# Performance work log

Measured on AMD Instinct MI355X. Metric: run time of the kernel, lower is better.

Reference implementation:

```python
import jax, jax.numpy as jnp
import numpy as np

N_NODES = 100000


def setup_inputs() -> dict:
    key = jax.random.key(0)
    ks = jax.random.split(key, 7)
    feats = jax.random.normal(ks[0], (N_NODES, 128), dtype=jnp.float32)
    src = jax.random.randint(ks[1], (1000000,), 0, N_NODES)
    dst = jax.random.randint(ks[2], (1000000,), 0, N_NODES)
    W1 = jax.random.normal(ks[3], (128, 128), dtype=jnp.float32) * (1.0 / np.sqrt(128))
    b1 = jnp.zeros((128,), dtype=jnp.float32)
    W2 = jax.random.normal(ks[4], (128, 40), dtype=jnp.float32) * (1.0 / np.sqrt(128))
    b2 = jnp.zeros((40,), dtype=jnp.float32)
    return {"feats": feats, "src": src, "dst": dst, "W1": W1, "b1": b1, "W2": W2, "b2": b2}


def _sage_gcn_layer(h, src, dst, deg, W, b):
    # DGL SAGEConv aggregator_type='gcn':
    #   neigh = sum over in-edges of src features; h = (neigh + h_self) / (in_deg + 1); out = h @ W + b
    neigh = jax.ops.segment_sum(h[src], dst, num_segments=N_NODES)  # [N, d]
    agg = (neigh + h) / (deg[:, None] + 1.0)
    return agg @ W + b


def reference(feats, src, dst, W1, b1, W2, b2):
    deg = jax.ops.segment_sum(jnp.ones_like(dst, dtype=feats.dtype), dst, num_segments=N_NODES)
    h1 = jax.nn.relu(_sage_gcn_layer(feats, src, dst, deg, W1, b1))  # dropout = identity (eval)
    h2 = _sage_gcn_layer(h1, src, dst, deg, W2, b2)
    # original returns (h_list, h); h_list = [h1, h2], final h = h2
    return (h1, h2)
```

## Files before the change

kernel.cpp:

```cpp
#include <hip/hip_runtime.h>

static inline int ceil_div(int a, int b){ return (a+b-1)/b; }

__global__ __launch_bounds__(256) void k_hist(const int* __restrict__ dst, int E, int* __restrict__ cnt){
  int e = blockIdx.x*256 + threadIdx.x;
  if (e < E) atomicAdd(&cnt[dst[e]], 1);
}

__global__ __launch_bounds__(256) void k_scan_a(const int* __restrict__ cnt, int N, int* __restrict__ bsum){
  __shared__ int s[256];
  int t = threadIdx.x;
  int i0 = blockIdx.x*512 + 2*t;
  int a = (i0   < N) ? cnt[i0]   : 0;
  int b = (i0+1 < N) ? cnt[i0+1] : 0;
  s[t] = a + b;
  __syncthreads();
  for (int off=128; off>0; off>>=1){ if (t<off) s[t]+=s[t+off]; __syncthreads(); }
  if (t==0) bsum[blockIdx.x] = s[0];
}

__global__ __launch_bounds__(256) void k_scan_b(int* __restrict__ bsum, int nb){
  __shared__ int s[256];
  int t = threadIdx.x;
  int v0=0,v1=0,v2=0,v3=0;
  int i0 = t*4;
  if (i0   < nb) v0 = bsum[i0];
  if (i0+1 < nb) v1 = bsum[i0+1];
  if (i0+2 < nb) v2 = bsum[i0+2];
  if (i0+3 < nb) v3 = bsum[i0+3];
  int tsum = v0+v1+v2+v3;
  s[t] = tsum;
  __syncthreads();
  for (int off=1; off<256; off<<=1){
    int v = (t>=off) ? s[t-off] : 0;
    __syncthreads();
    s[t] += v;
    __syncthreads();
  }
  int excl = s[t] - tsum;
  if (i0   < nb) bsum[i0]   = excl;
  if (i0+1 < nb) bsum[i0+1] = excl + v0;
  if (i0+2 < nb) bsum[i0+2] = excl + v0 + v1;
  if (i0+3 < nb) bsum[i0+3] = excl + v0 + v1 + v2;
}

__global__ __launch_bounds__(256) void k_scan_c(const int* __restrict__ cnt, int N,
                                                const int* __restrict__ bsum, int* __restrict__ offs){
  __shared__ int s[256];
  int t = threadIdx.x;
  int i0 = blockIdx.x*512 + 2*t;
  int a = (i0   < N) ? cnt[i0]   : 0;
  int b = (i0+1 < N) ? cnt[i0+1] : 0;
  int tsum = a+b;
  s[t] = tsum;
  __syncthreads();
  for (int off=1; off<256; off<<=1){
    int v = (t>=off) ? s[t-off] : 0;
    __syncthreads();
    s[t] += v;
    __syncthreads();
  }
  int excl = s[t] - tsum + bsum[blockIdx.x];
  if (i0   < N) offs[i0]   = excl;
  if (i0+1 < N) offs[i0+1] = excl + a;
}

__global__ __launch_bounds__(256) void k_place(const int* __restrict__ src, const int* __restrict__ dst, int E,
                                               const int* __restrict__ offs, int* __restrict__ cursor,
                                               int* __restrict__ ss){
  int e = blockIdx.x*256 + threadIdx.x;
  if (e < E){
    int d = dst[e];
    int p = atomicAdd(&cursor[d], 1);
    ss[offs[d] + p] = src[e];
  }
}

__global__ __launch_bounds__(256) void k_agg1(const float* __restrict__ feats,
    const int* __restrict__ ss, const int* __restrict__ offs, const int* __restrict__ cnt,
    float* __restrict__ aggout, int N){
  int w = (int)((blockIdx.x*256u + threadIdx.x) >> 6);
  int lane = threadIdx.x & 63;
  if (w >= N) return;
  int beg = __builtin_amdgcn_readfirstlane(offs[w]);
  int c   = __builtin_amdgcn_readfirstlane(cnt[w]);
  const float2* f2 = (const float2*)feats;
  float2 acc = f2[(size_t)w*64 + lane];
  int i = 0;
  for (; i+4 <= c; i += 4){
    int s0 = ss[beg+i], s1 = ss[beg+i+1], s2 = ss[beg+i+2], s3 = ss[beg+i+3];
    float2 a = f2[(size_t)s0*64 + lane];
    float2 b = f2[(size_t)s1*64 + lane];
    float2 cc= f2[(size_t)s2*64 + lane];
    float2 d = f2[(size_t)s3*64 + lane];
    acc.x += (a.x + b.x) + (cc.x + d.x);
    acc.y += (a.y + b.y) + (cc.y + d.y);
  }
  for (; i < c; ++i){
    int s0 = ss[beg+i];
    float2 a = f2[(size_t)s0*64 + lane];
    acc.x += a.x; acc.y += a.y;
  }
  float inv = 1.0f / (float)(c + 1);
  float2 o; o.x = acc.x*inv; o.y = acc.y*inv;
  ((float2*)aggout)[(size_t)w*64 + lane] = o;
}

__global__ __launch_bounds__(256) void k_gemm1(float* __restrict__ h1,
    const float* __restrict__ W1, const float* __restrict__ b1, int N){
  __shared__ float sA[64*132];
  __shared__ float sW[32*128];
  int t = threadIdx.x;
  int r0 = blockIdx.x*64;
  for (int it=0; it<8; ++it){
    int flat = it*1024 + t*4;
    int r = flat>>7, d = flat&127;
    float4 v = make_float4(0.f,0.f,0.f,0.f);
    if (r0+r < N) v = *(const float4*)(h1 + (size_t)(r0+r)*128 + d);
    *(float4*)&sA[r*132 + d] = v;
  }
  int rg = t>>4, cg = t&15;
  float acc[4][8];
#pragma unroll
  for (int i=0;i<4;++i)
#pragma unroll
    for (int j=0;j<8;++j) acc[i][j]=0.f;

  for (int kc=0; kc<4; ++kc){
    __syncthreads();
#pragma unroll
    for (int it=0; it<4; ++it){
      int flat = it*1024 + t*4;
      *(float4*)&sW[flat] = *(const float4*)(W1 + kc*4096 + flat);
    }
    __syncthreads();
#pragma unroll 4
    for (int dd=0; dd<32; ++dd){
      int d = kc*32 + dd;
      float4 w0 = *(const float4*)&sW[dd*128 + cg*4];
      float4 w1 = *(const float4*)&sW[dd*128 + 64 + cg*4];
      float a0 = sA[(rg   )*132 + d];
      float a1 = sA[(rg+16)*132 + d];
      float a2 = sA[(rg+32)*132 + d];
      float a3 = sA[(rg+48)*132 + d];
      acc[0][0]+=a0*w0.x; acc[0][1]+=a0*w0.y; acc[0][2]+=a0*w0.z; acc[0][3]+=a0*w0.w;
      acc[0][4]+=a0*w1.x; acc[0][5]+=a0*w1.y; acc[0][6]+=a0*w1.z; acc[0][7]+=a0*w1.w;
      acc[1][0]+=a1*w0.x; acc[1][1]+=a1*w0.y; acc[1][2]+=a1*w0.z; acc[1][3]+=a1*w0.w;
      acc[1][4]+=a1*w1.x; acc[1][5]+=a1*w1.y; acc[1][6]+=a1*w1.z; acc[1][7]+=a1*w1.w;
      acc[2][0]+=a2*w0.x; acc[2][1]+=a2*w0.y; acc[2][2]+=a2*w0.z; acc[2][3]+=a2*w0.w;
      acc[2][4]+=a2*w1.x; acc[2][5]+=a2*w1.y; acc[2][6]+=a2*w1.z; acc[2][7]+=a2*w1.w;
      acc[3][0]+=a3*w0.x; acc[3][1]+=a3*w0.y; acc[3][2]+=a3*w0.z; acc[3][3]+=a3*w0.w;
      acc[3][4]+=a3*w1.x; acc[3][5]+=a3*w1.y; acc[3][6]+=a3*w1.z; acc[3][7]+=a3*w1.w;
    }
  }
  float4 bb0 = *(const float4*)(b1 + cg*4);
  float4 bb1 = *(const float4*)(b1 + 64 + cg*4);
#pragma unroll
  for (int i=0;i<4;++i){
    int r = r0 + rg + i*16;
    if (r < N){
      float4 o0, o1;
      o0.x = fmaxf(acc[i][0]+bb0.x, 0.f); o0.y = fmaxf(acc[i][1]+bb0.y, 0.f);
      o0.z = fmaxf(acc[i][2]+bb0.z, 0.f); o0.w = fmaxf(acc[i][3]+bb0.w, 0.f);
      o1.x = fmaxf(acc[i][4]+bb1.x, 0.f); o1.y = fmaxf(acc[i][5]+bb1.y, 0.f);
      o1.z = fmaxf(acc[i][6]+bb1.z, 0.f); o1.w = fmaxf(acc[i][7]+bb1.w, 0.f);
      *(float4*)(h1 + (size_t)r*128 + cg*4)      = o0;
      *(float4*)(h1 + (size_t)r*128 + 64 + cg*4) = o1;
    }
  }
}

__global__ __launch_bounds__(256) void k_gemm2(const float* __restrict__ h1,
    const float* __restrict__ W2, float* __restrict__ t1, int N){
  __shared__ float sA[64*132];
  __shared__ float sW[128*40];
  int t = threadIdx.x;
  int r0 = blockIdx.x*64;
  for (int it=0; it<8; ++it){
    int flat = it*1024 + t*4;
    int r = flat>>7, d = flat&127;
    float4 v = make_float4(0.f,0.f,0.f,0.f);
    if (r0+r < N) v = *(const float4*)(h1 + (size_t)(r0+r)*128 + d);
    *(float4*)&sA[r*132 + d] = v;
  }
#pragma unroll
  for (int it=0; it<5; ++it){
    int flat = it*1024 + t*4;
    *(float4*)&sW[flat] = *(const float4*)(W2 + flat);
  }
  __syncthreads();
  int rg = t>>3, cg = t&7;
  float acc[2][5];
#pragma unroll
  for (int i=0;i<2;++i)
#pragma unroll
    for (int j=0;j<5;++j) acc[i][j]=0.f;
#pragma unroll 4
  for (int d=0; d<128; ++d){
    float a0 = sA[(rg   )*132 + d];
    float a1 = sA[(rg+32)*132 + d];
#pragma unroll
    for (int jj=0;jj<5;++jj){
      float wv = sW[d*40 + cg + 8*jj];
      acc[0][jj] += a0*wv;
      acc[1][jj] += a1*wv;
    }
  }
#pragma unroll
  for (int i=0;i<2;++i){
    int r = r0 + rg + i*32;
    if (r < N){
#pragma unroll
      for (int jj=0;jj<5;++jj) t1[(size_t)r*40 + cg + 8*jj] = acc[i][jj];
    }
  }
}

__global__ __launch_bounds__(256) void k_agg2(const float* __restrict__ t1,
    const int* __restrict__ ss, const int* __restrict__ offs, const int* __restrict__ cnt,
    const float* __restrict__ b2, float* __restrict__ h2, int N){
  int w = (int)((blockIdx.x*256u + threadIdx.x) >> 6);
  int lane = threadIdx.x & 63;
  if (w >= N) return;
  int beg = __builtin_amdgcn_readfirstlane(offs[w]);
  int c   = __builtin_amdgcn_readfirstlane(cnt[w]);
  int l = (lane < 40) ? lane : 0;
  float acc = t1[(size_t)w*40 + l];
  int i = 0;
  for (; i+4 <= c; i += 4){
    int s0 = ss[beg+i], s1 = ss[beg+i+1], s2 = ss[beg+i+2], s3 = ss[beg+i+3];
    float a = t1[(size_t)s0*40 + l];
    float b = t1[(size_t)s1*40 + l];
    float cc= t1[(size_t)s2*40 + l];
    float d = t1[(size_t)s3*40 + l];
    acc += (a + b) + (cc + d);
  }
  for (; i < c; ++i) acc += t1[(size_t)ss[beg+i]*40 + l];
  float inv = 1.0f / (float)(c + 1);
  if (lane < 40) h2[(size_t)w*40 + lane] = acc*inv + b2[lane];
}

extern "C" void kernel_launch(void* const* d_in, const int* in_sizes, int n_in,
                              void* d_out, int out_size, void* d_ws, size_t ws_size,
                              hipStream_t stream){
  const float* feats = (const float*)d_in[0];
  const int*   src   = (const int*)d_in[1];
  const int*   dst   = (const int*)d_in[2];
  const float* W1    = (const float*)d_in[3];
  const float* b1    = (const float*)d_in[4];
  const float* W2    = (const float*)d_in[5];
  const float* b2    = (const float*)d_in[6];
  int N = in_sizes[0] / 128;
  int E = in_sizes[1];
  float* h1 = (float*)d_out;
  float* h2 = h1 + (size_t)N*128;

  size_t need = 0;
  auto lay = [&](size_t bytes)->size_t{ size_t p = need; need += (bytes + 511) & ~(size_t)511; return p; };
  size_t o_cnt    = lay((size_t)N*4);
  size_t o_offs   = lay((size_t)N*4);
  size_t o_cursor = lay((size_t)N*4);
  size_t o_bsum   = lay(4096);
  size_t o_ss     = lay((size_t)E*4);
  size_t o_t1     = lay((size_t)N*40*4);
  if (need > ws_size) return;

  char* wp = (char*)d_ws;
  int*   cnt    = (int*)(wp + o_cnt);
  int*   offs   = (int*)(wp + o_offs);
  int*   cursor = (int*)(wp + o_cursor);
  int*   bsum   = (int*)(wp + o_bsum);
  int*   ss     = (int*)(wp + o_ss);
  float* t1     = (float*)(wp + o_t1);

  hipMemsetAsync(cnt,    0, (size_t)N*4, stream);
  hipMemsetAsync(cursor, 0, (size_t)N*4, stream);

  int nb = ceil_div(N, 512);
  k_hist  <<<ceil_div(E,256), 256, 0, stream>>>(dst, E, cnt);
  k_scan_a<<<nb,              256, 0, stream>>>(cnt, N, bsum);
  k_scan_b<<<1,               256, 0, stream>>>(bsum, nb);
  k_scan_c<<<nb,              256, 0, stream>>>(cnt, N, bsum, offs);
  k_place <<<ceil_div(E,256), 256, 0, stream>>>(src, dst, E, offs, cursor, ss);

  k_agg1  <<<ceil_div(N,4),   256, 0, stream>>>(feats, ss, offs, cnt, h1, N);
  k_gemm1 <<<ceil_div(N,64),  256, 0, stream>>>(h1, W1, b1, N);
  k_gemm2 <<<ceil_div(N,64),  256, 0, stream>>>(h1, W2, t1, N);
  k_agg2  <<<ceil_div(N,4),   256, 0, stream>>>(t1, ss, offs, cnt, b2, h2, N);
}
```

Baseline: 413.3 us.

## Fuse the two GEMMs, drop the cursor array, widen layer-1 gather to float4

k_place now bumps the offsets array atomically, so the separate cursor buffer and its memset go away; the aggregation kernels recover each segment's start as offs minus count. k_agg1 gathers with float4 loads, with each half-wave handling alternate edges and a shuffle merging the two halves. k_gemm1 and k_gemm2 become one kernel that keeps the relu'd h1 tile in shared memory for the second product, which avoids re-reading h1 from global memory. The cost is more shared-memory reuse and a less regular tail in the gather loop.

```diff
diff --git a/kernel.cpp b/kernel.cpp
--- a/kernel.cpp
+++ b/kernel.cpp
@@ -66,13 +66,12 @@
 }
 
 __global__ __launch_bounds__(256) void k_place(const int* __restrict__ src, const int* __restrict__ dst, int E,
-                                               const int* __restrict__ offs, int* __restrict__ cursor,
-                                               int* __restrict__ ss){
+                                               int* __restrict__ offs, int* __restrict__ ss){
   int e = blockIdx.x*256 + threadIdx.x;
   if (e < E){
     int d = dst[e];
-    int p = atomicAdd(&cursor[d], 1);
-    ss[offs[d] + p] = src[e];
+    int p = atomicAdd(&offs[d], 1);
+    ss[p] = src[e];
   }
 }
 
@@ -82,34 +81,58 @@
   int w = (int)((blockIdx.x*256u + threadIdx.x) >> 6);
   int lane = threadIdx.x & 63;
   if (w >= N) return;
-  int beg = __builtin_amdgcn_readfirstlane(offs[w]);
   int c   = __builtin_amdgcn_readfirstlane(cnt[w]);
-  const float2* f2 = (const float2*)feats;
-  float2 acc = f2[(size_t)w*64 + lane];
+  int beg = __builtin_amdgcn_readfirstlane(offs[w]) - c;
+  const float4* f4 = (const float4*)feats;
+  int half = lane >> 5;
+  int qc   = lane & 31;
+  float4 acc = make_float4(0.f,0.f,0.f,0.f);
   int i = 0;
-  for (; i+4 <= c; i += 4){
-    int s0 = ss[beg+i], s1 = ss[beg+i+1], s2 = ss[beg+i+2], s3 = ss[beg+i+3];
-    float2 a = f2[(size_t)s0*64 + lane];
-    float2 b = f2[(size_t)s1*64 + lane];
-    float2 cc= f2[(size_t)s2*64 + lane];
-    float2 d = f2[(size_t)s3*64 + lane];
+  for (; i+8 <= c; i += 8){
+    int i0 = ss[beg+i  +half];
+    int i1 = ss[beg+i+2+half];
+    int i2 = ss[beg+i+4+half];
+    int i3 = ss[beg+i+6+half];
+    float4 a = f4[(size_t)i0*32 + qc];
+    float4 b = f4[(size_t)i1*32 + qc];
+    float4 cc= f4[(size_t)i2*32 + qc];
+    float4 d = f4[(size_t)i3*32 + qc];
     acc.x += (a.x + b.x) + (cc.x + d.x);
     acc.y += (a.y + b.y) + (cc.y + d.y);
-  }
-  for (; i < c; ++i){
-    int s0 = ss[beg+i];
-    float2 a = f2[(size_t)s0*64 + lane];
-    acc.x += a.x; acc.y += a.y;
-  }
-  float inv = 1.0f / (float)(c + 1);
-  float2 o; o.x = acc.x*inv; o.y = acc.y*inv;
-  ((float2*)aggout)[(size_t)w*64 + lane] = o;
-}
-
-__global__ __launch_bounds__(256) void k_gemm1(float* __restrict__ h1,
-    const float* __restrict__ W1, const float* __restrict__ b1, int N){
+    acc.z += (a.z + b.z) + (cc.z + d.z);
+    acc.w += (a.w + b.w) + (cc.w + d.w);
+  }
+  for (; i+2 <= c; i += 2){
+    int i0 = ss[beg+i+half];
+    float4 a = f4[(size_t)i0*32 + qc];
+    acc.x += a.x; acc.y += a.y; acc.z += a.z; acc.w += a.w;
+  }
+  acc.x += __shfl_down(acc.x, 32, 64);
+  acc.y += __shfl_down(acc.y, 32, 64);
+  acc.z += __shfl_down(acc.z, 32, 64);
+  acc.w += __shfl_down(acc.w, 32, 64);
+  if (lane < 32){
+    if (i < c){
+      int i0 = ss[beg+i];
+      float4 a = f4[(size_t)i0*32 + qc];
+      acc.x += a.x; acc.y += a.y; acc.z += a.z; acc.w += a.w;
+    }
+    float4 s = f4[(size_t)w*32 + qc];
+    float inv = 1.0f / (float)(c + 1);
+    float4 o;
+    o.x = (acc.x + s.x) * inv;
+    o.y = (acc.y + s.y) * inv;
+    o.z = (acc.z + s.z) * inv;
+    o.w = (acc.w + s.w) * inv;
+    ((float4*)aggout)[(size_t)w*32 + qc] = o;
+  }
+}
+
+__global__ __launch_bounds__(256) void k_gemm12(float* __restrict__ h1,
+    const float* __restrict__ W1, const float* __restrict__ b1,
+    const float* __restrict__ W2, float* __restrict__ t1, int N){
   __shared__ float sA[64*132];
-  __shared__ float sW[32*128];
+  __shared__ float sW[5120];
   int t = threadIdx.x;
   int r0 = blockIdx.x*64;
   for (int it=0; it<8; ++it){
@@ -153,35 +176,25 @@
       acc[3][4]+=a3*w1.x; acc[3][5]+=a3*w1.y; acc[3][6]+=a3*w1.z; acc[3][7]+=a3*w1.w;
     }
   }
+  __syncthreads();
+
   float4 bb0 = *(const float4*)(b1 + cg*4);
   float4 bb1 = *(const float4*)(b1 + 64 + cg*4);
 #pragma unroll
   for (int i=0;i<4;++i){
-    int r = r0 + rg + i*16;
+    int rr = rg + i*16;
+    int r  = r0 + rr;
+    float4 o0, o1;
+    o0.x = fmaxf(acc[i][0]+bb0.x, 0.f); o0.y = fmaxf(acc[i][1]+bb0.y, 0.f);
+    o0.z = fmaxf(acc[i][2]+bb0.z, 0.f); o0.w = fmaxf(acc[i][3]+bb0.w, 0.f);
+    o1.x = fmaxf(acc[i][4]+bb1.x, 0.f); o1.y = fmaxf(acc[i][5]+bb1.y, 0.f);
+    o1.z = fmaxf(acc[i][6]+bb1.z, 0.f); o1.w = fmaxf(acc[i][7]+bb1.w, 0.f);
+    *(float4*)&sA[rr*132 + cg*4]      = o0;
+    *(float4*)&sA[rr*132 + 64 + cg*4] = o1;
     if (r < N){
-      float4 o0, o1;
-      o0.x = fmaxf(acc[i][0]+bb0.x, 0.f); o0.y = fmaxf(acc[i][1]+bb0.y, 0.f);
-      o0.z = fmaxf(acc[i][2]+bb0.z, 0.f); o0.w = fmaxf(acc[i][3]+bb0.w, 0.f);
-      o1.x = fmaxf(acc[i][4]+bb1.x, 0.f); o1.y = fmaxf(acc[i][5]+bb1.y, 0.f);
-      o1.z = fmaxf(acc[i][6]+bb1.z, 0.f); o1.w = fmaxf(acc[i][7]+bb1.w, 0.f);
       *(float4*)(h1 + (size_t)r*128 + cg*4)      = o0;
       *(float4*)(h1 + (size_t)r*128 + 64 + cg*4) = o1;
     }
-  }
-}
-
-__global__ __launch_bounds__(256) void k_gemm2(const float* __restrict__ h1,
-    const float* __restrict__ W2, float* __restrict__ t1, int N){
-  __shared__ float sA[64*132];
-  __shared__ float sW[128*40];
-  int t = threadIdx.x;
-  int r0 = blockIdx.x*64;
-  for (int it=0; it<8; ++it){
-    int flat = it*1024 + t*4;
-    int r = flat>>7, d = flat&127;
-    float4 v = make_float4(0.f,0.f,0.f,0.f);
-    if (r0+r < N) v = *(const float4*)(h1 + (size_t)(r0+r)*128 + d);
-    *(float4*)&sA[r*132 + d] = v;
   }
 #pragma unroll
   for (int it=0; it<5; ++it){
@@ -189,29 +202,30 @@
     *(float4*)&sW[flat] = *(const float4*)(W2 + flat);
   }
   __syncthreads();
-  int rg = t>>3, cg = t&7;
-  float acc[2][5];
+
+  int rg2 = t>>3, cg2 = t&7;
+  float a2c[2][5];
 #pragma unroll
   for (int i=0;i<2;++i)
 #pragma unroll
-    for (int j=0;j<5;++j) acc[i][j]=0.f;
+    for (int j=0;j<5;++j) a2c[i][j]=0.f;
 #pragma unroll 4
   for (int d=0; d<128; ++d){
-    float a0 = sA[(rg   )*132 + d];
-    float a1 = sA[(rg+32)*132 + d];
+    float a0 = sA[(rg2   )*132 + d];
+    float a1 = sA[(rg2+32)*132 + d];
 #pragma unroll
     for (int jj=0;jj<5;++jj){
-      float wv = sW[d*40 + cg + 8*jj];
-      acc[0][jj] += a0*wv;
-      acc[1][jj] += a1*wv;
+      float wv = sW[d*40 + cg2 + 8*jj];
+      a2c[0][jj] += a0*wv;
+      a2c[1][jj] += a1*wv;
     }
   }
 #pragma unroll
   for (int i=0;i<2;++i){
-    int r = r0 + rg + i*32;
+    int r = r0 + rg2 + i*32;
     if (r < N){
 #pragma unroll
-      for (int jj=0;jj<5;++jj) t1[(size_t)r*40 + cg + 8*jj] = acc[i][jj];
+      for (int jj=0;jj<5;++jj) t1[(size_t)r*40 + cg2 + 8*jj] = a2c[i][jj];
     }
   }
 }
@@ -222,8 +236,8 @@
   int w = (int)((blockIdx.x*256u + threadIdx.x) >> 6);
   int lane = threadIdx.x & 63;
   if (w >= N) return;
-  int beg = __builtin_amdgcn_readfirstlane(offs[w]);
   int c   = __builtin_amdgcn_readfirstlane(cnt[w]);
+  int beg = __builtin_amdgcn_readfirstlane(offs[w]) - c;
   int l = (lane < 40) ? lane : 0;
   float acc = t1[(size_t)w*40 + l];
   int i = 0;
@@ -259,7 +273,6 @@
   auto lay = [&](size_t bytes)->size_t{ size_t p = need; need += (bytes + 511) & ~(size_t)511; return p; };
   size_t o_cnt    = lay((size_t)N*4);
   size_t o_offs   = lay((size_t)N*4);
-  size_t o_cursor = lay((size_t)N*4);
   size_t o_bsum   = lay(4096);
   size_t o_ss     = lay((size_t)E*4);
   size_t o_t1     = lay((size_t)N*40*4);
@@ -268,23 +281,20 @@
   char* wp = (char*)d_ws;
   int*   cnt    = (int*)(wp + o_cnt);
   int*   offs   = (int*)(wp + o_offs);
-  int*   cursor = (int*)(wp + o_cursor);
   int*   bsum   = (int*)(wp + o_bsum);
   int*   ss     = (int*)(wp + o_ss);
   float* t1     = (float*)(wp + o_t1);
 
-  hipMemsetAsync(cnt,    0, (size_t)N*4, stream);
-  hipMemsetAsync(cursor, 0, (size_t)N*4, stream);
+  hipMemsetAsync(cnt, 0, (size_t)N*4, stream);
 
   int nb = ceil_div(N, 512);
   k_hist  <<<ceil_div(E,256), 256, 0, stream>>>(dst, E, cnt);
   k_scan_a<<<nb,              256, 0, stream>>>(cnt, N, bsum);
   k_scan_b<<<1,               256, 0, stream>>>(bsum, nb);
   k_scan_c<<<nb,              256, 0, stream>>>(cnt, N, bsum, offs);
-  k_place <<<ceil_div(E,256), 256, 0, stream>>>(src, dst, E, offs, cursor, ss);
+  k_place <<<ceil_div(E,256), 256, 0, stream>>>(src, dst, E, offs, ss);
 
   k_agg1  <<<ceil_div(N,4),   256, 0, stream>>>(feats, ss, offs, cnt, h1, N);
-  k_gemm1 <<<ceil_div(N,64),  256, 0, stream>>>(h1, W1, b1, N);
-  k_gemm2 <<<ceil_div(N,64),  256, 0, stream>>>(h1, W2, t1, N);
+  k_gemm12<<<ceil_div(N,64),  256, 0, stream>>>(h1, W1, b1, W2, t1, N);
   k_agg2  <<<ceil_div(N,4),   256, 0, stream>>>(t1, ss, offs, cnt, b2, h2, N);
 }
```

Measured after the change: 425.0 us. 1.03x slower.
